# Performance work log

Measured on AMD Instinct MI355X. Metric: run time of the kernel, lower is better.

The kernel has to match this reference:

```python
import jax, jax.numpy as jnp
import numpy as np
from jax import lax

C = 128
HEADS = 4
WS = 7      # spatial search window (per side radius 3)
WT = 1      # temporal radius -> frames t-1..t+1
EPS = 1e-6

_R = WS // 2
OFFS = np.array([(dt, dh, dw)
                 for dt in range(-WT, WT + 1)
                 for dh in range(-_R, _R + 1)
                 for dw in range(-_R, _R + 1)], dtype=np.int32)  # [L,3]


def layernorm_c(x, g, b):
    # LayerNorm2D: normalize over channel dim of [B,T,C,H,W]
    mu = jnp.mean(x, axis=2, keepdims=True)
    var = jnp.var(x, axis=2, keepdims=True)
    xn = (x - mu) * lax.rsqrt(var + EPS)
    return xn * g[None, None, :, None, None] + b[None, None, :, None, None]


def conv2d(x, w, b):
    y = lax.conv_general_dilated(x, w, (1, 1), 'SAME',
                                 dimension_numbers=('NCHW', 'OIHW', 'NCHW'))
    return y + b[None, :, None, None]


def setup_inputs() -> dict:
    key = jax.random.key(0)
    ks = jax.random.split(key, 16)
    B, T, H, W = 1, 4, 128, 128
    vid = jax.random.normal(ks[0], (B, T, C, H, W), jnp.float32)
    flows = jax.random.normal(ks[1], (B, T, 2, H, W), jnp.float32)
    s = 1.0 / np.sqrt(C)
    Wq = jax.random.normal(ks[2], (C, C), jnp.float32) * s
    Wk = jax.random.normal(ks[3], (C, C), jnp.float32) * s
    Wv = jax.random.normal(ks[4], (C, C), jnp.float32) * s
    Wo = jax.random.normal(ks[5], (C, C), jnp.float32) * s
    g0 = jnp.ones((C,), jnp.float32); b0 = jnp.zeros((C,), jnp.float32)
    g1 = jnp.ones((C,), jnp.float32); b1 = jnp.zeros((C,), jnp.float32)
    sc = 1.0 / np.sqrt(C * 9)
    w_r1 = jax.random.normal(ks[6], (C, C, 3, 3), jnp.float32) * sc
    b_r1 = jnp.zeros((C,), jnp.float32)
    w_r2 = jax.random.normal(ks[7], (C, C, 3, 3), jnp.float32) * sc
    b_r2 = jnp.zeros((C,), jnp.float32)
    return dict(vid=vid, flows=flows, g0=g0, b0=b0, Wq=Wq, Wk=Wk, Wv=Wv, Wo=Wo,
                g1=g1, b1=b1, w_r1=w_r1, b_r1=b_r1, w_r2=w_r2, b_r2=b_r2)


def _forward(vid, flows, g0, b0, Wq, Wk, Wv, Wo, g1, b1, w_r1, b_r1, w_r2, b_r2):
    B, T, _, H, W = vid.shape
    hd = C // HEADS
    N = T * H * W
    scale = hd ** -0.5

    x = layernorm_c(vid, g0, b0)
    q = jnp.einsum('btchw,oc->btohw', x, Wq)
    k = jnp.einsum('btchw,oc->btohw', x, Wk)
    v = jnp.einsum('btchw,oc->btohw', x, Wv)
    qh = q.transpose(0, 1, 3, 4, 2).reshape(B, N, HEADS, hd)
    kf = k.transpose(0, 1, 3, 4, 2).reshape(B, N, C)
    vf = v.transpose(0, 1, 3, 4, 2).reshape(B, N, C)

    tt = jnp.arange(T)[:, None, None]
    hh = jnp.arange(H)[None, :, None]
    ww = jnp.arange(W)[None, None, :]
    fh = flows[:, :, 0]  # [B,T,H,W]
    fw = flows[:, :, 1]
    offs = jnp.asarray(OFFS)

    def score_body(_, off):
        dt, dh, dw = off[0], off[1], off[2]
        t_i = jnp.clip(tt + dt, 0, T - 1)                        # [T,H,W]
        oh = jnp.round(fh * dt).astype(jnp.int32)                 # flow-guided center
        ow = jnp.round(fw * dt).astype(jnp.int32)
        h_i = jnp.clip(hh[None] + oh + dh, 0, H - 1)              # [B,T,H,W]
        w_i = jnp.clip(ww[None] + ow + dw, 0, W - 1)
        flat = ((jnp.broadcast_to(t_i[None], (B, T, H, W)) * H + h_i) * W + w_i).reshape(B, N)
        kg = jnp.take_along_axis(kf, flat[:, :, None], axis=1).reshape(B, N, HEADS, hd)
        s = jnp.einsum('bnhd,bnhd->bnh', qh, kg) * scale
        return None, (s, flat)

    _, (scores, flats) = lax.scan(score_body, None, offs)         # [L,B,N,HD], [L,B,N]
    wts = jax.nn.softmax(scores, axis=0)

    def agg_body(acc, inp):
        wl, fl = inp
        vg = jnp.take_along_axis(vf, fl[:, :, None], axis=1).reshape(B, N, HEADS, hd)
        return acc + wl[..., None] * vg, None

    acc, _ = lax.scan(agg_body, jnp.zeros((B, N, HEADS, hd), vid.dtype), (wts, flats))
    attn = acc.reshape(B, T, H, W, C).transpose(0, 1, 4, 2, 3)
    attn = jnp.einsum('btchw,oc->btohw', attn, Wo)

    vid1 = vid + attn
    y = layernorm_c(vid1, g1, b1)
    yb = y.reshape(B * T, C, H, W)
    r = conv2d(yb, w_r1, b_r1)
    r = jax.nn.gelu(r)
    r = conv2d(r, w_r2, b_r2)
    res = (yb + r).reshape(B, T, C, H, W)
    return vid1 + res


def reference(vid, flows, g0, b0, Wq, Wk, Wv, Wo, g1, b1, w_r1, b_r1, w_r2, b_r2):
    return _forward(vid, flows, g0, b0, Wq, Wk, Wv, Wo, g1, b1, w_r1, b_r1, w_r2, b_r2)
```

## Files before the change

### kernel.cpp

```cpp
#include <hip/hip_runtime.h>

__device__ __forceinline__ float bflo(unsigned int u){ return __builtin_bit_cast(float, (unsigned int)(u<<16)); }
__device__ __forceinline__ float bfhi(unsigned int u){ return __builtin_bit_cast(float, (unsigned int)(u & 0xffff0000u)); }
__device__ __forceinline__ float b2f(unsigned short s){ return __builtin_bit_cast(float, ((unsigned int)s)<<16); }
__device__ __forceinline__ unsigned short f2b(float f){
  unsigned int x = __builtin_bit_cast(unsigned int, f);
  x += 0x7fffu + ((x>>16)&1u);
  return (unsigned short)(x>>16);
}
__device__ __forceinline__ unsigned int packbf(float a, float b){
  return (unsigned int)f2b(a) | ((unsigned int)f2b(b)<<16);
}
__device__ __forceinline__ unsigned short f2h(float f){
  return __builtin_bit_cast(unsigned short, (_Float16)f);
}
__device__ __forceinline__ float dpp_swap1(float s){
  int so = __builtin_amdgcn_mov_dpp(__builtin_bit_cast(int, s), 0xB1, 0xF, 0xF, true);
  return __builtin_bit_cast(float, so);
}
__device__ __forceinline__ unsigned swz(unsigned b){ return b ^ (((b>>8)&7u)<<4); }

using bf16x8 = __attribute__((ext_vector_type(8))) short;
using f32x4  = __attribute__((ext_vector_type(4))) float;
using f32x2  = __attribute__((ext_vector_type(2))) float;
using h2     = __attribute__((ext_vector_type(2))) _Float16;

__device__ __forceinline__ h2 uh(unsigned int u){ return __builtin_bit_cast(h2, u); }

#define NPOS 65536
#define SLOT_ELEMS 8388608
#define WM_OFF 6291456

__global__ __launch_bounds__(256) void k_wprep(const float* __restrict__ w1,
                                               const float* __restrict__ w2,
                                               const float* __restrict__ Wq,
                                               const float* __restrict__ Wk,
                                               const float* __restrict__ Wv,
                                               const float* __restrict__ Wo,
                                               unsigned short* __restrict__ o1,
                                               unsigned short* __restrict__ o2,
                                               unsigned short* __restrict__ wm){
  int idx = blockIdx.x*256 + threadIdx.x;
  if (idx < 147456){
    int o = idx / 1152;
    int rem = idx - o*1152;
    int c = rem / 9;
    int tap = rem - c*9;
    int dsti = tap*16384 + o*128 + c;
    o1[dsti] = f2b(w1[idx]);
    o2[dsti] = f2b(w2[idx]);
  } else if (idx < 212992){
    int idx2 = idx - 147456;
    int mat = idx2 >> 14;
    int ij  = idx2 & 16383;
    float v = (mat==0) ? Wq[ij]*0.2550348613f
            : (mat==1) ? Wk[ij]
            : (mat==2) ? Wv[ij] : Wo[ij];
    wm[idx2] = f2b(v);
  }
}

__global__ __launch_bounds__(256) void k_ln_nchw(const float* __restrict__ vid,
                                                 const float* __restrict__ g,
                                                 const float* __restrict__ b,
                                                 unsigned short* __restrict__ xf){
  int n = blockIdx.x*256 + threadIdx.x;
  int t = n >> 14, hw = n & 16383;
  const float* base = vid + (size_t)t*2097152 + hw;
  float s=0.f, ss=0.f;
  #pragma unroll 8
  for (int c=0;c<128;c++){ float v=base[(size_t)c*16384]; s+=v; ss+=v*v; }
  float mu  = s*0.0078125f;
  float var = fmaxf(ss*0.0078125f - mu*mu, 0.f);
  float rs  = rsqrtf(var + 1e-6f);
  unsigned int* op = (unsigned int*)(xf + (size_t)n*128);
  #pragma unroll 4
  for (int c=0;c<128;c+=2){
    float v0=(base[(size_t)c*16384]    -mu)*rs*g[c]  +b[c];
    float v1=(base[(size_t)(c+1)*16384]-mu)*rs*g[c+1]+b[c+1];
    op[c>>1]=packbf(v0,v1);
  }
}

__global__ __launch_bounds__(256) void k_ln_rows(const unsigned short* __restrict__ x,
                                                 const float* __restrict__ g,
                                                 const float* __restrict__ b,
                                                 unsigned short* __restrict__ y){
  int n = blockIdx.x*256 + threadIdx.x;
  const unsigned int* p = (const unsigned int*)(x + (size_t)n*128);
  float s=0.f, ss=0.f;
  #pragma unroll 8
  for (int j=0;j<64;j++){ unsigned int u=p[j]; float v0=bflo(u),v1=bfhi(u); s+=v0+v1; ss+=v0*v0+v1*v1; }
  float mu  = s*0.0078125f;
  float var = fmaxf(ss*0.0078125f - mu*mu, 0.f);
  float rs  = rsqrtf(var + 1e-6f);
  unsigned int* op=(unsigned int*)(y+(size_t)n*128);
  #pragma unroll 8
  for (int j=0;j<64;j++){
    unsigned int u=p[j];
    float v0=(bflo(u)-mu)*rs*g[2*j]  +b[2*j];
    float v1=(bfhi(u)-mu)*rs*g[2*j+1]+b[2*j+1];
    op[j]=packbf(v0,v1);
  }
}

__global__ __launch_bounds__(256) void k_qkv(const unsigned short* xf,
                                             const unsigned short* __restrict__ wm,
                                             unsigned short* qf,
                                             unsigned short* __restrict__ kfo,
                                             unsigned short* __restrict__ vfo){
  __shared__ unsigned short wlds[16384];
  int wave = threadIdx.x>>6, lane = threadIdx.x&63;
  int m0w = blockIdx.x*256 + wave*64;
  int mrow = lane&15, quad = lane>>4;
  #pragma unroll 1
  for (int mi=0; mi<3; mi++){
    int mat = 2-mi;
    __syncthreads();
    { const uint4* src=(const uint4*)(wm + mat*16384);
      #pragma unroll
      for (int i=0;i<8;i++){
        unsigned bb=(threadIdx.x+256*i)*16;
        *(uint4*)((char*)wlds + swz(bb)) = src[threadIdx.x+256*i];
      } }
    __syncthreads();
    #pragma unroll 1
    for (int mt=0; mt<4; mt++){
      int m0 = m0w + mt*16;
      bf16x8 a[4];
      const unsigned short* ap = xf + (size_t)(m0+mrow)*128 + quad*8;
      #pragma unroll
      for (int kc=0;kc<4;kc++) a[kc] = *(const bf16x8*)(ap + kc*32);
      for (int nt=0;nt<8;nt++){
        f32x4 acc = {0.f,0.f,0.f,0.f};
        #pragma unroll
        for (int kc=0;kc<4;kc++){
          bf16x8 bfr = *(const bf16x8*)((const char*)wlds + swz((nt*16+mrow)*256 + kc*64 + quad*16));
          acc = __builtin_amdgcn_mfma_f32_16x16x32_bf16(a[kc], bfr, acc, 0,0,0);
        }
        int col = nt*16+mrow;
        if (mat==2){
          unsigned char* op8 = (unsigned char*)vfo + (size_t)(m0 + quad*4)*128 + col;
          #pragma unroll
          for (int r=0;r<4;r++){
            int pk = __builtin_amdgcn_cvt_pk_fp8_f32(acc[r], acc[r], 0, false);
            op8[(size_t)r*128] = (unsigned char)(pk & 0xff);
          }
        } else {
          unsigned short* out = (mat==0) ? qf : kfo;
          unsigned short* op = out + (size_t)(m0 + quad*4)*128 + col;
          #pragma unroll
          for (int r=0;r<4;r++) op[(size_t)r*128] = f2h(acc[r]);
        }
      }
    }
  }
}

__global__ __launch_bounds__(256) void k_attn(const unsigned short* qf,
                                              const unsigned short* __restrict__ kf,
                                              const unsigned short* __restrict__ vf,
                                              const float* __restrict__ flw,
                                              unsigned short* attf){
  int xcd = blockIdx.x & 7;
  int j   = blockIdx.x >> 3;
  int t       = j >> 6;
  int r       = j & 63;
  int h_local = r >> 2;
  int wq      = r & 3;
  int h = xcd*16 + h_local;
  int w = wq*32 + (threadIdx.x >> 3);
  int head  = (threadIdx.x >> 1) & 3;
  int cpart = threadIdx.x & 1;
  int hw = (h<<7) + w;
  int n  = (t<<14) + hw;
  float fh = flw[t*32768 + hw];
  float fw = flw[t*32768 + 16384 + hw];
  unsigned coff = head*32 + cpart*16;
  const unsigned char* vf8 = (const unsigned char*)vf;
  const uint4* qp = (const uint4*)(qf + (size_t)n*128 + coff);
  uint4 q0v = qp[0], q1v = qp[1];
  unsigned qw[8] = {q0v.x,q0v.y,q0v.z,q0v.w,q1v.x,q1v.y,q1v.z,q1v.w};
  float acc[16];
  #pragma unroll
  for (int i=0;i<16;i++) acc[i]=0.f;
  float l = 0.f;

  int rowb0, rowb1, rowb2;
  int hb0, hb1, hb2;
  int wm30, wm31, wm32;
  int w0c0, w0c1, w0c2;
  {
    int ti;
    ti = t-1; ti = ti<0?0:ti;   rowb0 = ti<<14;
    rowb1 = t<<14;
    ti = t+1; ti = ti>3?3:ti;   rowb2 = ti<<14;
    int oh = (int)rintf(fh*(-1.0f)), ow = (int)rintf(fw*(-1.0f));
    hb0 = h+oh; wm30 = w+ow-3;
    hb1 = h;    wm31 = w-3;
    oh = (int)rintf(fh*(1.0f)); ow = (int)rintf(fw*(1.0f));
    hb2 = h+oh; wm32 = w+ow-3;
    w0c0 = wm30<0?0:(wm30>127?127:wm30);
    w0c1 = wm31<0?0:(wm31>127?127:wm31);
    w0c2 = wm32<0?0:(wm32>127?127:wm32);
  }

  uint4 ka0, ka1, va;
  {
    int hi0 = hb0-3; hi0 = hi0<0?0:(hi0>127?127:hi0);
    unsigned b0 = ((unsigned)(rowb0 + (hi0<<7) + w0c0)<<7) + coff;
    ka0 = ((const uint4*)(kf + b0))[0];
    ka1 = ((const uint4*)(kf + b0))[1];
    va  = *(const uint4*)(vf8 + b0);
  }

  #pragma unroll
  for (int x=0; x<3; x++){
    const int rb_t = (x==0)?rowb0:((x==1)?rowb1:rowb2);
    const int hb   = (x==0)?hb0:((x==1)?hb1:hb2);
    const int wm3  = (x==0)?wm30:((x==1)?wm31:wm32);
    const int w0c  = (x==0)?w0c0:((x==1)?w0c1:w0c2);
    const int nrb  = (x==0)?rowb1:rowb2;
    const int nhb  = (x==0)?hb1:hb2;
    const int nw0c = (x==0)?w0c1:w0c2;
    #pragma unroll 1
    for (int dh=-3; dh<=3; dh++){
      int hi = hb+dh; hi = hi<0?0:(hi>127?127:hi);
      int rbase = rb_t + (hi<<7);
      #pragma unroll
      for (int i=0;i<7;i++){
        unsigned bon;
        if (i<6){
          int wi = wm3+i+1; wi = wi<0?0:(wi>127?127:wi);
          bon = ((unsigned)(rbase + wi)<<7) + coff;
        } else if (dh<3){
          int hi2 = hb+dh+1; hi2 = hi2<0?0:(hi2>127?127:hi2);
          bon = ((unsigned)(rb_t + (hi2<<7) + w0c)<<7) + coff;
        } else if (x<2){
          int hi2 = nhb-3; hi2 = hi2<0?0:(hi2>127?127:hi2);
          bon = ((unsigned)(nrb + (hi2<<7) + nw0c)<<7) + coff;
        } else {
          bon = coff;
        }
        uint4 kb0 = ((const uint4*)(kf + bon))[0];
        uint4 kb1 = ((const uint4*)(kf + bon))[1];
        uint4 vb  = *(const uint4*)(vf8 + bon);
        float s0 = 0.f, s1 = 0.f;
        s0 = __builtin_amdgcn_fdot2(uh(qw[0]), uh(ka0.x), s0, false);
        s0 = __builtin_amdgcn_fdot2(uh(qw[1]), uh(ka0.y), s0, false);
        s0 = __builtin_amdgcn_fdot2(uh(qw[2]), uh(ka0.z), s0, false);
        s0 = __builtin_amdgcn_fdot2(uh(qw[3]), uh(ka0.w), s0, false);
        s1 = __builtin_amdgcn_fdot2(uh(qw[4]), uh(ka1.x), s1, false);
        s1 = __builtin_amdgcn_fdot2(uh(qw[5]), uh(ka1.y), s1, false);
        s1 = __builtin_amdgcn_fdot2(uh(qw[6]), uh(ka1.z), s1, false);
        s1 = __builtin_amdgcn_fdot2(uh(qw[7]), uh(ka1.w), s1, false);
        float s = s0 + s1;
        s += dpp_swap1(s);
        float e = exp2f(s);
        l += e;
        f32x2 c0 = __builtin_amdgcn_cvt_pk_f32_fp8((int)va.x, false);
        f32x2 c1 = __builtin_amdgcn_cvt_pk_f32_fp8((int)va.x, true);
        f32x2 c2 = __builtin_amdgcn_cvt_pk_f32_fp8((int)va.y, false);
        f32x2 c3 = __builtin_amdgcn_cvt_pk_f32_fp8((int)va.y, true);
        f32x2 c4 = __builtin_amdgcn_cvt_pk_f32_fp8((int)va.z, false);
        f32x2 c5 = __builtin_amdgcn_cvt_pk_f32_fp8((int)va.z, true);
        f32x2 c6 = __builtin_amdgcn_cvt_pk_f32_fp8((int)va.w, false);
        f32x2 c7 = __builtin_amdgcn_cvt_pk_f32_fp8((int)va.w, true);
        acc[0]  += e*c0.x; acc[1]  += e*c0.y;
        acc[2]  += e*c1.x; acc[3]  += e*c1.y;
        acc[4]  += e*c2.x; acc[5]  += e*c2.y;
        acc[6]  += e*c3.x; acc[7]  += e*c3.y;
        acc[8]  += e*c4.x; acc[9]  += e*c4.y;
        acc[10] += e*c5.x; acc[11] += e*c5.y;
        acc[12] += e*c6.x; acc[13] += e*c6.y;
        acc[14] += e*c7.x; acc[15] += e*c7.y;
        ka0=kb0; ka1=kb1; va=vb;
      }
    }
  }
  float inv = 1.f/l;
  unsigned int* op = (unsigned int*)(attf + (size_t)n*128 + coff);
  #pragma unroll
  for (int i=0;i<8;i++) op[i]=packbf(acc[2*i]*inv, acc[2*i+1]*inv);
}

__global__ __launch_bounds__(256) void k_wo(const unsigned short* attf,
                                            const unsigned short* __restrict__ wm,
                                            const float* __restrict__ vid,
                                            unsigned short* vid1){
  __shared__ unsigned short wlds[16384];
  int wave = threadIdx.x>>6, lane = threadIdx.x&63;
  int m0w = blockIdx.x*256 + wave*64;
  int mrow = lane&15, quad = lane>>4;
  { const uint4* src=(const uint4*)(wm + 49152);
    #pragma unroll
    for (int i=0;i<8;i++){
      unsigned bb=(threadIdx.x+256*i)*16;
      *(uint4*)((char*)wlds + swz(bb)) = src[threadIdx.x+256*i];
    } }
  __syncthreads();
  #pragma unroll 1
  for (int mt=0; mt<4; mt++){
    int m0 = m0w + mt*16;
    bf16x8 a[4];
    const unsigned short* ap = attf + (size_t)(m0+mrow)*128 + quad*8;
    #pragma unroll
    for (int kc=0;kc<4;kc++) a[kc] = *(const bf16x8*)(ap + kc*32);
    for (int nt=0;nt<8;nt++){
      f32x4 acc={0.f,0.f,0.f,0.f};
      #pragma unroll
      for (int kc=0;kc<4;kc++){
        bf16x8 bfr = *(const bf16x8*)((const char*)wlds + swz((nt*16+mrow)*256 + kc*64 + quad*16));
        acc = __builtin_amdgcn_mfma_f32_16x16x32_bf16(a[kc], bfr, acc, 0,0,0);
      }
      int col = nt*16+mrow;
      #pragma unroll
      for (int r=0;r<4;r++){
        int nrow = m0 + quad*4 + r;
        int tt = nrow>>14, hww = nrow&16383;
        float resid = vid[(size_t)tt*2097152 + (size_t)col*16384 + hww];
        vid1[(size_t)nrow*128 + col] = f2b(resid + acc[r]);
      }
    }
  }
}

#define CONV_PROLOG \
  __shared__ unsigned short wlds[8192]; \
  int wv = threadIdx.x>>6, lane = threadIdx.x&63; \
  int mrow = lane&15, quad = lane>>4; \
  int chalf = blockIdx.x & 1; \
  int h = (blockIdx.x>>1) & 127; \
  int frame = blockIdx.x>>8; \
  size_t nf = (size_t)frame*16384; \
  f32x4 accA[4], accB[4]; \
  _Pragma("unroll") \
  for (int i=0;i<4;i++){ accA[i]=(f32x4){0.f,0.f,0.f,0.f}; accB[i]=(f32x4){0.f,0.f,0.f,0.f}; } \
  { const uint4* sp=(const uint4*)(wtap + chalf*8192); \
    uint4 s0=sp[threadIdx.x], s1=sp[threadIdx.x+256], s2=sp[threadIdx.x+512], s3=sp[threadIdx.x+768]; \
    unsigned b0=(unsigned)threadIdx.x*16; \
    *(uint4*)((char*)wlds + swz(b0))         = s0; \
    *(uint4*)((char*)wlds + swz(b0+4096u))   = s1; \
    *(uint4*)((char*)wlds + swz(b0+8192u))   = s2; \
    *(uint4*)((char*)wlds + swz(b0+12288u))  = s3; } \
  __syncthreads(); \
  _Pragma("unroll 1") \
  for (int tap=0; tap<9; tap++){ \
    uint4 s0,s1,s2,s3; \
    if (tap<8){ const uint4* sp=(const uint4*)(wtap + (size_t)(tap+1)*16384 + chalf*8192); \
      s0=sp[threadIdx.x]; s1=sp[threadIdx.x+256]; s2=sp[threadIdx.x+512]; s3=sp[threadIdx.x+768]; } \
    int ky=tap/3, kx=tap-3*ky; \
    int h2c=h+ky-1; \
    if ((unsigned)h2c<128u){ \
      int wA = wv*32 + mrow + kx - 1;             \
      int wAc = wA < 0 ? 0 : wA; \
      int wB = wA + 16;                           \
      int wBc = wB > 127 ? 127 : wB; \
      const unsigned short* rowp = src + (nf + (size_t)h2c*128)*128 + quad*8; \
      const unsigned short* apA = rowp + (size_t)wAc*128; \
      const unsigned short* apB = rowp + (size_t)wBc*128; \
      bf16x8 aA[4], aB[4]; \
      _Pragma("unroll") \
      for (int kc=0;kc<4;kc++){ aA[kc]=*(const bf16x8*)(apA+kc*32); aB[kc]=*(const bf16x8*)(apB+kc*32); } \
      if (kx==0 && wv==0 && mrow==0){ _Pragma("unroll") for (int kc=0;kc<4;kc++) aA[kc]=(bf16x8){0,0,0,0,0,0,0,0}; } \
      if (kx==2 && wv==3 && mrow==15){ _Pragma("unroll") for (int kc=0;kc<4;kc++) aB[kc]=(bf16x8){0,0,0,0,0,0,0,0}; } \
      _Pragma("unroll") \
      for (int nt=0;nt<4;nt++){ \
        _Pragma("unroll") \
        for (int kc=0;kc<4;kc++){ \
          bf16x8 bfr=*(const bf16x8*)((const char*)wlds + swz((nt*16+mrow)*256 + kc*64 + quad*16)); \
          accA[nt]=__builtin_amdgcn_mfma_f32_16x16x32_bf16(aA[kc],bfr,accA[nt],0,0,0); \
          accB[nt]=__builtin_amdgcn_mfma_f32_16x16x32_bf16(aB[kc],bfr,accB[nt],0,0,0); \
        } \
      } \
    } \
    __syncthreads(); \
    if (tap<8){ unsigned b0=(unsigned)threadIdx.x*16; \
      *(uint4*)((char*)wlds + swz(b0))         = s0; \
      *(uint4*)((char*)wlds + swz(b0+4096u))   = s1; \
      *(uint4*)((char*)wlds + swz(b0+8192u))   = s2; \
      *(uint4*)((char*)wlds + swz(b0+12288u))  = s3; \
      __syncthreads(); } \
  }

__global__ __launch_bounds__(256) void k_conv_gelu(const unsigned short* __restrict__ src,
                                                   const unsigned short* __restrict__ wtap,
                                                   const float* __restrict__ bias,
                                                   unsigned short* __restrict__ dst){
  CONV_PROLOG
  #pragma unroll
  for (int nt=0;nt<4;nt++){
    int col = chalf*64 + nt*16 + mrow;
    float bb = bias[col];
    #pragma unroll
    for (int r=0;r<4;r++){
      int pA = h*128 + wv*32 + quad*4 + r;
      float xA = accA[nt][r]+bb;
      float zA = 0.7978845608028654f*(xA+0.044715f*xA*xA*xA);
      dst[(nf+(size_t)pA)*128+col] = f2b(xA * __builtin_amdgcn_rcpf(1.f + __expf(-2.f*zA)));
      float xB = accB[nt][r]+bb;
      float zB = 0.7978845608028654f*(xB+0.044715f*xB*xB*xB);
      dst[(nf+(size_t)(pA+16))*128+col] = f2b(xB * __builtin_amdgcn_rcpf(1.f + __expf(-2.f*zB)));
    }
  }
}

__global__ __launch_bounds__(256) void k_conv_final(const unsigned short* __restrict__ src,
                                                    const unsigned short* __restrict__ wtap,
                                                    const float* __restrict__ bias,
                                                    const unsigned short* __restrict__ yb,
                                                    const unsigned short* __restrict__ vid1,
                                                    float* __restrict__ out){
  CONV_PROLOG
  #pragma unroll
  for (int nt=0;nt<4;nt++){
    int col = chalf*64 + nt*16 + mrow;
    float bb = bias[col];
    #pragma unroll
    for (int r=0;r<4;r++){
      int pA = h*128 + wv*32 + quad*4 + r;
      size_t rowA = nf+(size_t)pA, rowB = rowA+16;
      float xA = accA[nt][r]+bb;
      out[(size_t)frame*2097152 + (size_t)col*16384 + pA] =
        b2f(vid1[rowA*128+col]) + b2f(yb[rowA*128+col]) + xA;
      float xB = accB[nt][r]+bb;
      out[(size_t)frame*2097152 + (size_t)col*16384 + pA + 16] =
        b2f(vid1[rowB*128+col]) + b2f(yb[rowB*128+col]) + xB;
    }
  }
}

extern "C" void kernel_launch(void* const* d_in, const int* in_sizes, int n_in,
                              void* d_out, int out_size, void* d_ws, size_t ws_size,
                              hipStream_t stream) {
  const float* vid  = (const float*)d_in[0];
  const float* flw  = (const float*)d_in[1];
  const float* g0   = (const float*)d_in[2];
  const float* b0   = (const float*)d_in[3];
  const float* Wq   = (const float*)d_in[4];
  const float* Wk   = (const float*)d_in[5];
  const float* Wv   = (const float*)d_in[6];
  const float* Wo   = (const float*)d_in[7];
  const float* g1   = (const float*)d_in[8];
  const float* b1   = (const float*)d_in[9];
  const float* wr1  = (const float*)d_in[10];
  const float* br1  = (const float*)d_in[11];
  const float* wr2  = (const float*)d_in[12];
  const float* br2  = (const float*)d_in[13];
  float* out = (float*)d_out;

  unsigned short* A  = (unsigned short*)d_ws;
  unsigned short* Bs = A + SLOT_ELEMS;
  unsigned short* Cs = Bs + SLOT_ELEMS;
  bool four = ws_size >= (size_t)4*SLOT_ELEMS*2 + 2*294912;
  unsigned short* D  = four ? (Cs + SLOT_ELEMS) : A;
  unsigned short* wt1 = Cs + SLOT_ELEMS + (four ? SLOT_ELEMS : 0);
  unsigned short* wt2 = wt1 + 147456;
  unsigned short* wm  = Cs + WM_OFF;

  k_wprep   <<<832, 256, 0, stream>>>(wr1, wr2, Wq, Wk, Wv, Wo, wt1, wt2, wm);
  k_ln_nchw <<<256, 256, 0, stream>>>(vid, g0, b0, A);
  k_qkv     <<<256, 256, 0, stream>>>(A, wm, D, Bs, Cs);
  k_attn    <<<2048,256, 0, stream>>>(D, Bs, Cs, flw, D);
  k_wo      <<<256, 256, 0, stream>>>(D, wm, vid, D);
  k_ln_rows <<<256, 256, 0, stream>>>(D, g1, b1, Bs);
  k_conv_gelu <<<1024,256,0, stream>>>(Bs, wt1, br1, Cs);
  k_conv_final<<<1024,256,0, stream>>>(Cs, wt2, br2, Bs, D, out);
}
```

Before: 445.5 us.

## Stage conv input rows in LDS with register-prefetched double buffering

The 3x3 conv kernels now load each input row (128 pixels x 128 channels bf16) into shared memory once per ky and read the A fragments for all three kx taps from LDS, instead of issuing three separate global gathers. The next row is prefetched into registers during the current ky's last tap and written to LDS after the barrier, alongside the weight-tap prefetch. This cuts redundant global/L2 traffic for overlapping taps. In exchange it adds 32 KB of LDS per block, which may reduce occupancy, and uses more registers for the prefetch buffer.

```diff
diff --git a/kernel.cpp b/kernel.cpp
--- a/kernel.cpp
+++ b/kernel.cpp
@@ -327,6 +327,7 @@
 
 #define CONV_PROLOG \
   __shared__ unsigned short wlds[8192]; \
+  __shared__ unsigned short inlds[16384]; \
   int wv = threadIdx.x>>6, lane = threadIdx.x&63; \
   int mrow = lane&15, quad = lane>>4; \
   int chalf = blockIdx.x & 1; \
@@ -342,45 +343,61 @@
     *(uint4*)((char*)wlds + swz(b0))         = s0; \
     *(uint4*)((char*)wlds + swz(b0+4096u))   = s1; \
     *(uint4*)((char*)wlds + swz(b0+8192u))   = s2; \
-    *(uint4*)((char*)wlds + swz(b0+12288u))  = s3; } \
+    *(uint4*)((char*)wlds + swz(b0+12288u))  = s3; \
+    if (h>=1){ const uint4* ip=(const uint4*)(src + (nf + (size_t)(h-1)*128)*128); \
+      _Pragma("unroll") \
+      for (int j2=0;j2<8;j2++) \
+        *(uint4*)((char*)inlds + swz((unsigned)(threadIdx.x+256*j2)*16)) = ip[threadIdx.x+256*j2]; } } \
   __syncthreads(); \
   _Pragma("unroll 1") \
-  for (int tap=0; tap<9; tap++){ \
-    uint4 s0,s1,s2,s3; \
-    if (tap<8){ const uint4* sp=(const uint4*)(wtap + (size_t)(tap+1)*16384 + chalf*8192); \
-      s0=sp[threadIdx.x]; s1=sp[threadIdx.x+256]; s2=sp[threadIdx.x+512]; s3=sp[threadIdx.x+768]; } \
-    int ky=tap/3, kx=tap-3*ky; \
-    int h2c=h+ky-1; \
-    if ((unsigned)h2c<128u){ \
-      int wA = wv*32 + mrow + kx - 1;             \
-      int wAc = wA < 0 ? 0 : wA; \
-      int wB = wA + 16;                           \
-      int wBc = wB > 127 ? 127 : wB; \
-      const unsigned short* rowp = src + (nf + (size_t)h2c*128)*128 + quad*8; \
-      const unsigned short* apA = rowp + (size_t)wAc*128; \
-      const unsigned short* apB = rowp + (size_t)wBc*128; \
-      bf16x8 aA[4], aB[4]; \
-      _Pragma("unroll") \
-      for (int kc=0;kc<4;kc++){ aA[kc]=*(const bf16x8*)(apA+kc*32); aB[kc]=*(const bf16x8*)(apB+kc*32); } \
-      if (kx==0 && wv==0 && mrow==0){ _Pragma("unroll") for (int kc=0;kc<4;kc++) aA[kc]=(bf16x8){0,0,0,0,0,0,0,0}; } \
-      if (kx==2 && wv==3 && mrow==15){ _Pragma("unroll") for (int kc=0;kc<4;kc++) aB[kc]=(bf16x8){0,0,0,0,0,0,0,0}; } \
-      _Pragma("unroll") \
-      for (int nt=0;nt<4;nt++){ \
+  for (int ky=0; ky<3; ky++){ \
+    int h2c = h+ky-1; \
+    bool vld = (unsigned)h2c<128u; \
+    _Pragma("unroll 1") \
+    for (int kx=0; kx<3; kx++){ \
+      int tap = ky*3+kx; \
+      uint4 s0,s1,s2,s3; \
+      if (tap<8){ const uint4* sp=(const uint4*)(wtap + (size_t)(tap+1)*16384 + chalf*8192); \
+        s0=sp[threadIdx.x]; s1=sp[threadIdx.x+256]; s2=sp[threadIdx.x+512]; s3=sp[threadIdx.x+768]; } \
+      uint4 tr[8]; \
+      bool stg = (kx==2) && (ky<2) && (h+ky<128); \
+      if (stg){ const uint4* ip=(const uint4*)(src + (nf + (size_t)(h+ky)*128)*128); \
+        _Pragma("unroll") \
+        for (int j2=0;j2<8;j2++) tr[j2]=ip[threadIdx.x+256*j2]; } \
+      if (vld){ \
+        int wA = wv*32 + mrow + kx - 1;             \
+        int wAc = wA < 0 ? 0 : wA; \
+        int wB = wA + 16;                           \
+        int wBc = wB > 127 ? 127 : wB; \
+        bf16x8 aA[4], aB[4]; \
         _Pragma("unroll") \
         for (int kc=0;kc<4;kc++){ \
-          bf16x8 bfr=*(const bf16x8*)((const char*)wlds + swz((nt*16+mrow)*256 + kc*64 + quad*16)); \
-          accA[nt]=__builtin_amdgcn_mfma_f32_16x16x32_bf16(aA[kc],bfr,accA[nt],0,0,0); \
-          accB[nt]=__builtin_amdgcn_mfma_f32_16x16x32_bf16(aB[kc],bfr,accB[nt],0,0,0); \
+          aA[kc]=*(const bf16x8*)((const char*)inlds + swz((unsigned)(wAc*256 + kc*64 + quad*16))); \
+          aB[kc]=*(const bf16x8*)((const char*)inlds + swz((unsigned)(wBc*256 + kc*64 + quad*16))); } \
+        if (kx==0 && wv==0 && mrow==0){ _Pragma("unroll") for (int kc=0;kc<4;kc++) aA[kc]=(bf16x8){0,0,0,0,0,0,0,0}; } \
+        if (kx==2 && wv==3 && mrow==15){ _Pragma("unroll") for (int kc=0;kc<4;kc++) aB[kc]=(bf16x8){0,0,0,0,0,0,0,0}; } \
+        _Pragma("unroll") \
+        for (int nt=0;nt<4;nt++){ \
+          _Pragma("unroll") \
+          for (int kc=0;kc<4;kc++){ \
+            bf16x8 bfr=*(const bf16x8*)((const char*)wlds + swz((nt*16+mrow)*256 + kc*64 + quad*16)); \
+            accA[nt]=__builtin_amdgcn_mfma_f32_16x16x32_bf16(aA[kc],bfr,accA[nt],0,0,0); \
+            accB[nt]=__builtin_amdgcn_mfma_f32_16x16x32_bf16(aB[kc],bfr,accB[nt],0,0,0); \
+          } \
         } \
       } \
+      __syncthreads(); \
+      if (tap<8){ unsigned b0=(unsigned)threadIdx.x*16; \
+        *(uint4*)((char*)wlds + swz(b0))         = s0; \
+        *(uint4*)((char*)wlds + swz(b0+4096u))   = s1; \
+        *(uint4*)((char*)wlds + swz(b0+8192u))   = s2; \
+        *(uint4*)((char*)wlds + swz(b0+12288u))  = s3; } \
+      if (stg){ \
+        _Pragma("unroll") \
+        for (int j2=0;j2<8;j2++) \
+          *(uint4*)((char*)inlds + swz((unsigned)(threadIdx.x+256*j2)*16)) = tr[j2]; } \
+      if (tap<8) __syncthreads(); \
     } \
-    __syncthreads(); \
-    if (tap<8){ unsigned b0=(unsigned)threadIdx.x*16; \
-      *(uint4*)((char*)wlds + swz(b0))         = s0; \
-      *(uint4*)((char*)wlds + swz(b0+4096u))   = s1; \
-      *(uint4*)((char*)wlds + swz(b0+8192u))   = s2; \
-      *(uint4*)((char*)wlds + swz(b0+12288u))  = s3; \
-      __syncthreads(); } \
   }
 
 __global__ __launch_bounds__(256) void k_conv_gelu(const unsigned short* __restrict__ src,
```

Result: faster. 434.8 us (-2.4%).
